# Optimization experiments

Hardware: AMD Instinct MI355X
Metric: run time of the kernel (lower is better)

Reference implementation:

```python
import jax, jax.numpy as jnp
import numpy as np


def setup_inputs() -> dict:
    key = jax.random.key(0)
    k1, k2 = jax.random.split(key)
    N, D = 8192, 200
    preds = jax.random.normal(k1, (N, 1, 1, D), dtype=jnp.float32)
    labels = jax.random.randint(k2, (N,), 0, 64, dtype=jnp.int64)
    return {"preds": preds, "labels": labels}


def reference(preds, labels):
    # preds: (N,1,1,200) -> flatten to (N,200); torch.dist is the L2 norm of the
    # elementwise difference over the whole tensor.
    N = preds.shape[0]
    x = preds.reshape(N, -1).astype(jnp.float32)
    sq = jnp.sum(x * x, axis=-1)                      # (N,)
    gram = x @ x.T                                    # (N,N)
    d2 = sq[:, None] + sq[None, :] - 2.0 * gram       # squared pairwise dist
    eye = jnp.eye(N, dtype=bool)
    # keep diagonal out of the sqrt (it is skipped by the i==j continue)
    d2_safe = jnp.where(eye, 1.0, jnp.maximum(d2, 0.0))
    dist = jnp.sqrt(d2_safe)                          # (N,N)
    sign = jnp.where(labels[:, None] == labels[None, :], 1.0, -1.0)
    sign = jnp.where(eye, 0.0, sign)
    # each pred_loss[i] is a (1,1,200) tensor filled with the scalar s_i,
    # so the final mean over the stack equals mean_i(s_i).
    per_i = jnp.sum(sign * dist, axis=1)              # (N,)
    return jnp.mean(per_i)
```

## Files before the change

### kernel.cpp

```cpp
#include <hip/hip_runtime.h>
#include <hip/hip_fp8.h>

#define N 8192
#define D 200
#define KP 232
#define NSTEP 7
#define TB 128
#define NT 64
#define TPP 65
#define NBLK (32 * TPP)
#define PANEL (TB * KP)
#define NCELL 256

typedef float f32x4 __attribute__((ext_vector_type(4)));
#define AS3 __attribute__((address_space(3)))
#define AS1 __attribute__((address_space(1)))

__global__ __launch_bounds__(256) void prep_kernel(
    const float* __restrict__ x, const int* __restrict__ labels,
    unsigned char* __restrict__ xb, float* __restrict__ sq,
    int* __restrict__ lab, double* __restrict__ cells) {
  if (blockIdx.x == 0) cells[threadIdx.x] = 0.0;
  int row = blockIdx.x * 4 + (threadIdx.x >> 6);
  int lane = threadIdx.x & 63;
  const float* xr = x + (size_t)row * D;
  unsigned char* xbr = xb + (size_t)row * KP;
  int k0 = lane * 4;
  float4 f = {0.f, 0.f, 0.f, 0.f};
  if (k0 < D) f = *(const float4*)(xr + k0);
  float s = 0.f;
  unsigned char q[4];
  float ff[4] = {f.x, f.y, f.z, f.w};
#pragma unroll
  for (int c = 0; c < 4; ++c) {
    float v = (k0 + c < D) ? ff[c] : 0.f;
    __hip_fp8_e4m3 h(v);
    q[c] = h.__x;
    float fb = (float)h;
    s += fb * fb;
  }
  if (k0 < KP) *(uchar4*)(xbr + k0) = *(uchar4*)q;
#pragma unroll
  for (int m = 32; m; m >>= 1) s += __shfl_xor(s, m);
  if (lane == 0) {
    sq[row] = s;
    lab[row] = labels[row];
  }
}

__global__ __launch_bounds__(256, 2) void gram_kernel(
    const unsigned char* __restrict__ xb, const float* __restrict__ sq,
    const int* __restrict__ lab, double* __restrict__ cells) {
  __shared__ __align__(16) unsigned char sA[PANEL];
  __shared__ __align__(16) unsigned char sB[PANEL];

  const int t = threadIdx.x;
  const int b = (blockIdx.x & 7) * (NBLK / 8) + (blockIdx.x >> 3);
  const int q = b / TPP, idx = b - q * TPP;
  const int n1 = NT - q;
  const int I = (idx < n1) ? q : NT - 1 - q;
  const int J = (idx < n1) ? q + idx : (NT - 1 - q) + (idx - n1);

  auto stage = [&](const unsigned char* g, unsigned char* sh) {
#pragma unroll
    for (int c = 0; c < 7; ++c) {
      int off = c * 4096 + t * 16;
      __builtin_amdgcn_global_load_lds((const AS1 void*)(g + off),
                                       (AS3 void*)(sh + off), 16, 0, 0);
    }
    if (t < 64) {
      int off = 28672 + t * 16;
      __builtin_amdgcn_global_load_lds((const AS1 void*)(g + off),
                                       (AS3 void*)(sh + off), 16, 0, 0);
    }
  };
  stage(xb + (size_t)I * PANEL, sA);
  stage(xb + (size_t)J * PANEL, sB);

  const int wid = t >> 6, lane = t & 63;
  const int col = lane & 15, quad = lane >> 4;
  const int waveM = (wid >> 1) * 64, waveN = (wid & 1) * 64;
  const int i0 = I * TB + waveM, j0 = J * TB + waveN;
  int labj[4];
  float sqj[4];
#pragma unroll
  for (int ni = 0; ni < 4; ++ni) {
    int j = j0 + ni * 16 + col;
    labj[ni] = lab[j];
    sqj[ni] = sq[j];
  }
  float4 sqi4[4];
  int4 li4[4];
#pragma unroll
  for (int mi = 0; mi < 4; ++mi) {
    sqi4[mi] = *(const float4*)(sq + i0 + mi * 16 + quad * 4);
    li4[mi] = *(const int4*)(lab + i0 + mi * 16 + quad * 4);
  }
  __syncthreads();

  f32x4 acc[4][4] = {};
  __builtin_amdgcn_s_setprio(1);
#pragma unroll
  for (int step = 0; step < NSTEP; ++step) {
    long a[4], bf[4];
#pragma unroll
    for (int mi = 0; mi < 4; ++mi)
      a[mi] = *(const long*)(sA + (waveM + mi * 16 + col) * KP + step * 32 + quad * 8);
#pragma unroll
    for (int ni = 0; ni < 4; ++ni)
      bf[ni] = *(const long*)(sB + (waveN + ni * 16 + col) * KP + step * 32 + quad * 8);
#pragma unroll
    for (int mi = 0; mi < 4; ++mi)
#pragma unroll
      for (int ni = 0; ni < 4; ++ni)
        acc[mi][ni] = __builtin_amdgcn_mfma_f32_16x16x32_fp8_fp8(
            a[mi], bf[ni], acc[mi][ni], 0, 0, 0);
  }
  __builtin_amdgcn_s_setprio(0);

  float rs = 0.f, tot;
  if (I != J) {
#pragma unroll
    for (int mi = 0; mi < 4; ++mi) {
      float sqi[4] = {sqi4[mi].x, sqi4[mi].y, sqi4[mi].z, sqi4[mi].w};
      int li[4] = {li4[mi].x, li4[mi].y, li4[mi].z, li4[mi].w};
#pragma unroll
      for (int r = 0; r < 4; ++r)
#pragma unroll
        for (int ni = 0; ni < 4; ++ni) {
          float g = acc[mi][ni][r];
          float d2 = fmaxf(fmaf(-2.f, g, sqi[r] + sqj[ni]), 0.f);
          float dist = __builtin_amdgcn_sqrtf(d2);
          rs += (li[r] == labj[ni]) ? dist : -dist;
        }
    }
    tot = 2.f * rs;
  } else {
#pragma unroll
    for (int mi = 0; mi < 4; ++mi) {
      float sqi[4] = {sqi4[mi].x, sqi4[mi].y, sqi4[mi].z, sqi4[mi].w};
      int li[4] = {li4[mi].x, li4[mi].y, li4[mi].z, li4[mi].w};
#pragma unroll
      for (int r = 0; r < 4; ++r) {
        int i = i0 + mi * 16 + quad * 4 + r;
#pragma unroll
        for (int ni = 0; ni < 4; ++ni) {
          int j = j0 + ni * 16 + col;
          float g = acc[mi][ni][r];
          float d2 = fmaxf(fmaf(-2.f, g, sqi[r] + sqj[ni]), 0.f);
          float dist = __builtin_amdgcn_sqrtf(d2);
          float c = (li[r] == labj[ni]) ? dist : -dist;
          rs += (i == j) ? 0.f : c;
        }
      }
    }
    tot = rs;
  }

#pragma unroll
  for (int m = 32; m; m >>= 1) tot += __shfl_xor(tot, m);
  if (lane == 0)
    atomicAdd(&cells[(b * 4 + wid) & (NCELL - 1)], (double)tot);
}

__global__ __launch_bounds__(256) void reduce_kernel(
    const double* __restrict__ cells, float* __restrict__ out) {
  __shared__ double wsum[4];
  double s = cells[threadIdx.x];
#pragma unroll
  for (int m = 32; m; m >>= 1) s += __shfl_xor(s, m);
  if ((threadIdx.x & 63) == 0) wsum[threadIdx.x >> 6] = s;
  __syncthreads();
  if (threadIdx.x == 0)
    out[0] = (float)((wsum[0] + wsum[1] + wsum[2] + wsum[3]) / (double)N);
}

extern "C" void kernel_launch(void* const* d_in, const int* in_sizes, int n_in,
                              void* d_out, int out_size, void* d_ws, size_t ws_size,
                              hipStream_t stream) {
  const float* x = (const float*)d_in[0];
  const int* labels = (const int*)d_in[1];
  char* ws = (char*)d_ws;
  unsigned char* xb = (unsigned char*)ws;
  float* sq = (float*)(ws + (size_t)N * KP);
  int* lab = (int*)(ws + (size_t)N * KP + (size_t)N * 4);
  double* cells = (double*)(ws + (size_t)N * KP + (size_t)N * 8);
  float* out = (float*)d_out;

  prep_kernel<<<N / 4, 256, 0, stream>>>(x, labels, xb, sq, lab, cells);
  gram_kernel<<<NBLK, 256, 0, stream>>>(xb, sq, lab, cells);
  reduce_kernel<<<1, 256, 0, stream>>>(cells, out);
}
```

Measured before the change: 82.44 us.

## Store fp8 operands in MFMA-fragment-major layout and stagger block starts

Prep now writes the quantized matrix in a per-16-row, per-k-step fragment-major layout so each lane's 8-byte MFMA operand is contiguous. LDS reads become linear, which is meant to avoid bank conflicts from the old padded row stride, and the stage tail load disappears. Half of the blocks also execute a short s_sleep at start, apparently to stagger memory traffic, at the cost of some idle time.

Result: slower. 85.35 us (+3.5%).

```diff
diff --git a/kernel.cpp b/kernel.cpp
--- a/kernel.cpp
+++ b/kernel.cpp
@@ -3,13 +3,16 @@
 
 #define N 8192
 #define D 200
-#define KP 232
 #define NSTEP 7
 #define TB 128
 #define NT 64
 #define TPP 65
 #define NBLK (32 * TPP)
-#define PANEL (TB * KP)
+#define FSTEP 512
+#define PSTRIDE (NSTEP * FSTEP)
+#define PANEL_T (8 * PSTRIDE)
+#define NPANEL (N / 16)
+#define XBSZ ((size_t)NPANEL * PSTRIDE)
 #define NCELL 256
 
 typedef float f32x4 __attribute__((ext_vector_type(4)));
@@ -24,7 +27,6 @@
   int row = blockIdx.x * 4 + (threadIdx.x >> 6);
   int lane = threadIdx.x & 63;
   const float* xr = x + (size_t)row * D;
-  unsigned char* xbr = xb + (size_t)row * KP;
   int k0 = lane * 4;
   float4 f = {0.f, 0.f, 0.f, 0.f};
   if (k0 < D) f = *(const float4*)(xr + k0);
@@ -39,7 +41,14 @@
     float fb = (float)h;
     s += fb * fb;
   }
-  if (k0 < KP) *(uchar4*)(xbr + k0) = *(uchar4*)q;
+  if (k0 < NSTEP * 32) {
+    unsigned char* dst = xb + (size_t)(row >> 4) * PSTRIDE
+                       + (k0 >> 5) * FSTEP
+                       + ((k0 & 31) >> 3) * 128
+                       + (row & 15) * 8
+                       + (k0 & 7);
+    *(uchar4*)dst = *(uchar4*)q;
+  }
 #pragma unroll
   for (int m = 32; m; m >>= 1) s += __shfl_xor(s, m);
   if (lane == 0) {
@@ -51,8 +60,11 @@
 __global__ __launch_bounds__(256, 2) void gram_kernel(
     const unsigned char* __restrict__ xb, const float* __restrict__ sq,
     const int* __restrict__ lab, double* __restrict__ cells) {
-  __shared__ __align__(16) unsigned char sA[PANEL];
-  __shared__ __align__(16) unsigned char sB[PANEL];
+  __shared__ __align__(16) unsigned char sA[PANEL_T];
+  __shared__ __align__(16) unsigned char sB[PANEL_T];
+
+  if ((blockIdx.x >> 8) & 1)
+    __builtin_amdgcn_s_sleep(40);
 
   const int t = threadIdx.x;
   const int b = (blockIdx.x & 7) * (NBLK / 8) + (blockIdx.x >> 3);
@@ -68,14 +80,9 @@
       __builtin_amdgcn_global_load_lds((const AS1 void*)(g + off),
                                        (AS3 void*)(sh + off), 16, 0, 0);
     }
-    if (t < 64) {
-      int off = 28672 + t * 16;
-      __builtin_amdgcn_global_load_lds((const AS1 void*)(g + off),
-                                       (AS3 void*)(sh + off), 16, 0, 0);
-    }
   };
-  stage(xb + (size_t)I * PANEL, sA);
-  stage(xb + (size_t)J * PANEL, sB);
+  stage(xb + (size_t)(8 * I) * PSTRIDE, sA);
+  stage(xb + (size_t)(8 * J) * PSTRIDE, sB);
 
   const int wid = t >> 6, lane = t & 63;
   const int col = lane & 15, quad = lane >> 4;
@@ -98,6 +105,8 @@
   }
   __syncthreads();
 
+  const int pA = (waveM >> 4) * PSTRIDE + lane * 8;
+  const int pB = (waveN >> 4) * PSTRIDE + lane * 8;
   f32x4 acc[4][4] = {};
   __builtin_amdgcn_s_setprio(1);
 #pragma unroll
@@ -105,10 +114,10 @@
     long a[4], bf[4];
 #pragma unroll
     for (int mi = 0; mi < 4; ++mi)
-      a[mi] = *(const long*)(sA + (waveM + mi * 16 + col) * KP + step * 32 + quad * 8);
+      a[mi] = *(const long*)(sA + pA + mi * PSTRIDE + step * FSTEP);
 #pragma unroll
     for (int ni = 0; ni < 4; ++ni)
-      bf[ni] = *(const long*)(sB + (waveN + ni * 16 + col) * KP + step * 32 + quad * 8);
+      bf[ni] = *(const long*)(sB + pB + ni * PSTRIDE + step * FSTEP);
 #pragma unroll
     for (int mi = 0; mi < 4; ++mi)
 #pragma unroll
@@ -182,9 +191,9 @@
   const int* labels = (const int*)d_in[1];
   char* ws = (char*)d_ws;
   unsigned char* xb = (unsigned char*)ws;
-  float* sq = (float*)(ws + (size_t)N * KP);
-  int* lab = (int*)(ws + (size_t)N * KP + (size_t)N * 4);
-  double* cells = (double*)(ws + (size_t)N * KP + (size_t)N * 8);
+  float* sq = (float*)(ws + XBSZ);
+  int* lab = (int*)(ws + XBSZ + (size_t)N * 4);
+  double* cells = (double*)(ws + XBSZ + (size_t)N * 8);
   float* out = (float*)d_out;
 
   prep_kernel<<<N / 4, 256, 0, stream>>>(x, labels, xb, sq, lab, cells);
```
